# Kernel tuning notes

Measured on AMD Instinct MI355X. Metric: run time of the kernel, lower is better.

## Reference

```python
import jax, jax.numpy as jnp
import numpy as np

N_NODES = 100000
N_EDGES = 3200000
N_GRAPHS = 64


def gcn_conv(x, W, b, src, dst, num_nodes):
    # PyG GCNConv: h = x @ W; add self-loops; symmetric norm D^-1/2 (A+I) D^-1/2; bias after aggregation
    h = x @ W  # [N, out]
    loop = jnp.arange(num_nodes, dtype=src.dtype)
    src2 = jnp.concatenate([src, loop])
    dst2 = jnp.concatenate([dst, loop])
    deg = jax.ops.segment_sum(jnp.ones_like(src2, dtype=h.dtype), dst2, num_segments=num_nodes)
    dinv = jnp.where(deg > 0, jax.lax.rsqrt(jnp.maximum(deg, 1e-12)), 0.0)
    norm = dinv[src2] * dinv[dst2]  # [E+N]
    msg = h[src2] * norm[:, None]   # gather + scale (memory-bound)
    out = jax.ops.segment_sum(msg, dst2, num_segments=num_nodes)  # scatter-add
    return out + b


def global_mean_pool(x, batch, num_graphs):
    sums = jax.ops.segment_sum(x, batch, num_segments=num_graphs)
    cnts = jax.ops.segment_sum(jnp.ones((x.shape[0],), dtype=x.dtype), batch, num_segments=num_graphs)
    return sums / jnp.maximum(cnts, 1.0)[:, None]


def setup_inputs() -> dict:
    key = jax.random.key(0)
    ks = jax.random.split(key, 9)
    x = jax.random.normal(ks[0], (N_NODES, 1), dtype=jnp.float32)
    edge_index = jax.random.randint(ks[1], (2, N_EDGES), 0, N_NODES, dtype=jnp.int64)
    batch = jnp.sort(jax.random.randint(ks[2], (N_NODES,), 0, N_GRAPHS, dtype=jnp.int64))
    # Glorot-ish params
    W1 = jax.random.normal(ks[3], (1, 64), dtype=jnp.float32) * 0.5
    b1 = jnp.zeros((64,), dtype=jnp.float32)
    W2 = jax.random.normal(ks[4], (64, 32), dtype=jnp.float32) * (1.0 / np.sqrt(64))
    b2 = jnp.zeros((32,), dtype=jnp.float32)
    Wfc = jax.random.normal(ks[5], (32, 1), dtype=jnp.float32) * (1.0 / np.sqrt(32))
    bfc = jnp.zeros((1,), dtype=jnp.float32)
    return {"x": x, "edge_index": edge_index, "batch": batch,
            "W1": W1, "b1": b1, "W2": W2, "b2": b2, "Wfc": Wfc, "bfc": bfc}


def reference(x, edge_index, batch, W1, b1, W2, b2, Wfc, bfc):
    src, dst = edge_index[0], edge_index[1]
    h = jax.nn.relu(gcn_conv(x, W1, b1, src, dst, N_NODES))
    h = jax.nn.relu(gcn_conv(h, W2, b2, src, dst, N_NODES))
    g = global_mean_pool(h, batch, N_GRAPHS)  # [num_graphs, 32]
    return jax.nn.sigmoid(g @ Wfc + bfc)      # [num_graphs, 1]
```

## Files before the change

kernel.cpp:

```cpp
#include <hip/hip_runtime.h>
#include <math.h>

#define N_NODES 100000
#define N_EDGES 3200000
#define N_GRAPHS 64
#define BW 512
#define LSH 9
#define LMASK 511u
#define NBUCK ((N_NODES + BW - 1) / BW)
#define CHUNK_E 8192
#define NCHUNK ((N_EDGES + CHUNK_E - 1) / CHUNK_E)
#define POOL_SCALE 1024.0f
#define POOL_INV (1.0f / 1024.0f)
#define SENT ((unsigned int)N_NODES << LSH)

__global__ void k_count(const int* __restrict__ dst, unsigned int* __restrict__ counts,
                        unsigned int* __restrict__ totals) {
    __shared__ unsigned int h[NBUCK];
    for (int i = threadIdx.x; i < NBUCK; i += blockDim.x) h[i] = 0u;
    __syncthreads();
    int e0 = blockIdx.x * CHUNK_E;
    int e1 = min(e0 + CHUNK_E, N_EDGES);
    for (int e = e0 + threadIdx.x; e < e1; e += blockDim.x)
        atomicAdd(&h[dst[e] >> LSH], 1u);
    __syncthreads();
    for (int i = threadIdx.x; i < NBUCK; i += blockDim.x) {
        counts[(size_t)blockIdx.x * NBUCK + i] = h[i];
        if (h[i]) atomicAdd(&totals[i], h[i]);
    }
}

__global__ void k_scanc(unsigned int* __restrict__ counts, const unsigned int* __restrict__ totals,
                        unsigned int* __restrict__ base) {
    __shared__ unsigned int sd[1024];
    __shared__ unsigned int sbase;
    int bk = blockIdx.x;
    int t = threadIdx.x;
    unsigned int tv = (t < NBUCK) ? totals[t] : 0u;
    sd[t] = tv;
    __syncthreads();
    for (int o = 1; o < 1024; o <<= 1) {
        unsigned int x = (t >= o) ? sd[t - o] : 0u;
        __syncthreads();
        sd[t] += x;
        __syncthreads();
    }
    if (t == bk) {
        sbase = sd[t] - tv;
        base[bk] = sd[t] - tv;
        if (bk == 0) base[NBUCK] = N_EDGES;
    }
    __syncthreads();
    unsigned int v = (t < NCHUNK) ? counts[(size_t)t * NBUCK + bk] : 0u;
    sd[t] = v;
    __syncthreads();
    for (int o = 1; o < 1024; o <<= 1) {
        unsigned int x = (t >= o) ? sd[t - o] : 0u;
        __syncthreads();
        sd[t] += x;
        __syncthreads();
    }
    if (t < NCHUNK) counts[(size_t)t * NBUCK + bk] = sbase + sd[t] - v;
}

__global__ void k_part(const int* __restrict__ src, const int* __restrict__ dst,
                       const unsigned int* __restrict__ counts, unsigned int* __restrict__ packed) {
    __shared__ unsigned int sstart[NBUCK];
    __shared__ unsigned int lcur[NBUCK];
    for (int i = threadIdx.x; i < NBUCK; i += blockDim.x) {
        sstart[i] = counts[(size_t)blockIdx.x * NBUCK + i];
        lcur[i] = 0u;
    }
    __syncthreads();
    int e0 = blockIdx.x * CHUNK_E;
    int e1 = min(e0 + CHUNK_E, N_EDGES);
    for (int e = e0 + threadIdx.x; e < e1; e += blockDim.x) {
        int d = dst[e];
        int bk = d >> LSH;
        unsigned int pos = sstart[bk] + atomicAdd(&lcur[bk], 1u);
        packed[pos] = ((unsigned int)src[e] << LSH) | ((unsigned int)d & LMASK);
    }
}

__global__ void k_sort(const unsigned int* __restrict__ base, const unsigned int* __restrict__ packed,
                       unsigned int* __restrict__ packed2, unsigned int* __restrict__ rowstart) {
    __shared__ unsigned int hist[BW];
    __shared__ unsigned int scan[BW];
    __shared__ unsigned int cur[BW];
    int b = blockIdx.x;
    unsigned int e0 = base[b], e1 = base[b + 1];
    if (threadIdx.x < BW) hist[threadIdx.x] = 0u;
    __syncthreads();
    for (unsigned int e = e0 + threadIdx.x; e < e1; e += blockDim.x)
        atomicAdd(&hist[packed[e] & LMASK], 1u);
    __syncthreads();
    if (threadIdx.x < BW) scan[threadIdx.x] = hist[threadIdx.x];
    __syncthreads();
    for (int o = 1; o < BW; o <<= 1) {
        unsigned int v = 0u;
        if (threadIdx.x < BW && threadIdx.x >= (unsigned)o) v = scan[threadIdx.x - o];
        __syncthreads();
        if (threadIdx.x < BW && threadIdx.x >= (unsigned)o) scan[threadIdx.x] += v;
        __syncthreads();
    }
    if (threadIdx.x < BW) {
        unsigned int excl = scan[threadIdx.x] - hist[threadIdx.x];
        cur[threadIdx.x] = excl;
        rowstart[b * BW + threadIdx.x] = e0 + excl;
    }
    __syncthreads();
    for (unsigned int e = e0 + threadIdx.x; e < e1; e += blockDim.x) {
        unsigned int p = packed[e];
        unsigned int pos = e0 + atomicAdd(&cur[p & LMASK], 1u);
        packed2[pos] = p;
    }
}

__global__ void k_dinv(const unsigned int* __restrict__ rowstart, const float* __restrict__ x,
                       float* __restrict__ dinv, float* __restrict__ s, float2* __restrict__ ac) {
    int n = blockIdx.x * blockDim.x + threadIdx.x;
    if (n == 0) ac[N_NODES] = make_float2(0.0f, 0.0f);
    if (n < N_NODES) {
        unsigned int deg = rowstart[n + 1] - rowstart[n];
        float di = 1.0f / sqrtf((float)(deg + 1u));
        dinv[n] = di;
        s[n] = x[n] * di;
    }
}

__global__ void k_gcnt(const int* __restrict__ batch, float* __restrict__ gcnt) {
    __shared__ int lb[N_GRAPHS + 1];
    int b = threadIdx.x;
    if (b <= N_GRAPHS) {
        int lo = 0, hi = N_NODES;
        while (lo < hi) {
            int mid = (lo + hi) >> 1;
            if (batch[mid] < b) lo = mid + 1; else hi = mid;
        }
        lb[b] = lo;
    }
    __syncthreads();
    if (b < N_GRAPHS) gcnt[b] = (float)(lb[b + 1] - lb[b]);
}

#define NB1 16
__global__ void k_l1(const unsigned int* __restrict__ rowstart, const unsigned int* __restrict__ packed2,
                     const float* __restrict__ dinv, const float* __restrict__ s,
                     float2* __restrict__ ac) {
    int g = threadIdx.x >> 5, k = threadIdx.x & 31;
    int b = blockIdx.x;
    for (int d = g; d < NB1; d += 8) {
        int n = b * NB1 + d;
        if (n >= N_NODES) break;
        unsigned int rs = rowstart[n], re = rowstart[n + 1];
        float sum = 0.0f;
        for (unsigned int e = rs + k; e < re; e += 32)
            sum += s[packed2[e] >> LSH];
        sum += __shfl_xor(sum, 1);
        sum += __shfl_xor(sum, 2);
        sum += __shfl_xor(sum, 4);
        sum += __shfl_xor(sum, 8);
        sum += __shfl_xor(sum, 16);
        if (k == 0) {
            float di = dinv[n];
            ac[n] = make_float2(di, di * di * (sum + s[n]));
        }
    }
}

#define NPW 8

#define EDGE_PAIR(P) { \
    float4 q_ = Epair4[(P)]; \
    H += fmaxf(fmaf(q_.y, w1j, q_.x * b1j), 0.0f); \
    H += fmaxf(fmaf(q_.w, w1j, q_.z * b1j), 0.0f); }

#define BLOCK16(P0) { \
    EDGE_PAIR((P0) + 0) EDGE_PAIR((P0) + 1) EDGE_PAIR((P0) + 2) EDGE_PAIR((P0) + 3) \
    EDGE_PAIR((P0) + 4) EDGE_PAIR((P0) + 5) EDGE_PAIR((P0) + 6) EDGE_PAIR((P0) + 7) }

__global__ __launch_bounds__(256, 6)
void k_l2(const unsigned int* __restrict__ rowstart, const unsigned int* __restrict__ packed2,
          const float2* __restrict__ ac,
          const float* __restrict__ W1, const float* __restrict__ b1,
          const float* __restrict__ W2, const float* __restrict__ b2,
          const int* __restrict__ batch, int* __restrict__ gsumi) {
    __shared__ float Hrow[4][64];
    __shared__ float4 Ebuf[4][32];
    const int lane = threadIdx.x & 63;
    const int wv   = threadIdx.x >> 6;
    const int k    = lane & 31;
    const int jh   = lane >> 5;
    const int j0   = jh * 32;

    const float w1j = W1[lane];
    const float b1j = b1[lane];
    const float b2k = b2[k];
    float w2c[32];
#pragma unroll
    for (int j = 0; j < 32; j++) w2c[j] = W2[(j0 + j) * 32 + k];

    float4* Epair4 = &Ebuf[wv][0];
    float2* Ewr    = (float2*)&Ebuf[wv][0];

    int n0 = (blockIdx.x * 4 + wv) * NPW;
    float racc = 0.0f;
    int curg = -1;
    for (int i = 0; i < NPW; i++) {
        int n = n0 + i;
        if (n >= N_NODES) break;
        unsigned int rs = rowstart[n], re = rowstart[n + 1];
        float2 acn = ac[n];
        float H = fmaxf(fmaf(acn.y, w1j, acn.x * b1j), 0.0f);
        unsigned int e0 = rs;
        while (e0 + 64u <= re) {
            unsigned int p = packed2[e0 + lane];
            Ewr[lane] = ac[p >> LSH];
            BLOCK16(0) BLOCK16(8) BLOCK16(16) BLOCK16(24)
            e0 += 64u;
        }
        unsigned int rem = re - e0;
        if (rem) {
            unsigned int idx = e0 + lane;
            unsigned int p = SENT;
            if (idx < re) p = packed2[idx];
            Ewr[lane] = ac[p >> LSH];
            switch ((rem + 15u) >> 4) {
                case 4: BLOCK16(24); [[fallthrough]];
                case 3: BLOCK16(16); [[fallthrough]];
                case 2: BLOCK16(8);  [[fallthrough]];
                case 1: BLOCK16(0);
            }
        }
        Hrow[wv][lane] = H;
        float accv = 0.0f;
#pragma unroll
        for (int jj = 0; jj < 8; jj++) {
            float4 hv = *(const float4*)&Hrow[wv][j0 + 4 * jj];
            accv += hv.x * w2c[4 * jj + 0] + hv.y * w2c[4 * jj + 1]
                  + hv.z * w2c[4 * jj + 2] + hv.w * w2c[4 * jj + 3];
        }
        accv += __shfl_xor(accv, 32);
        float v = fmaxf(fmaf(acn.x, accv, b2k), 0.0f);
        int gb = batch[n];
        if (gb != curg) {
            if (curg >= 0 && jh == 0)
                atomicAdd(&gsumi[curg * 32 + k], __float2int_rn(racc * POOL_SCALE));
            racc = 0.0f; curg = gb;
        }
        racc += v;
    }
    if (curg >= 0 && jh == 0)
        atomicAdd(&gsumi[curg * 32 + k], __float2int_rn(racc * POOL_SCALE));
}

__global__ void k_readout(const int* __restrict__ gsumi, const float* __restrict__ gcnt,
                          const float* __restrict__ Wfc, const float* __restrict__ bfc,
                          float* __restrict__ out) {
    int b = threadIdx.x;
    if (b < N_GRAPHS) {
        float inv = 1.0f / fmaxf(gcnt[b], 1.0f);
        float acc = bfc[0];
#pragma unroll
        for (int k = 0; k < 32; k++)
            acc += (float)gsumi[b * 32 + k] * POOL_INV * inv * Wfc[k];
        out[b] = 1.0f / (1.0f + expf(-acc));
    }
}

extern "C" void kernel_launch(void* const* d_in, const int* in_sizes, int n_in,
                              void* d_out, int out_size, void* d_ws, size_t ws_size,
                              hipStream_t stream) {
    const float* x    = (const float*)d_in[0];
    const int*   ei   = (const int*)d_in[1];
    const int*   batch= (const int*)d_in[2];
    const float* W1   = (const float*)d_in[3];
    const float* b1   = (const float*)d_in[4];
    const float* W2   = (const float*)d_in[5];
    const float* b2   = (const float*)d_in[6];
    const float* Wfc  = (const float*)d_in[7];
    const float* bfc  = (const float*)d_in[8];
    float* out = (float*)d_out;

    const int* srcIdx = ei;
    const int* dstIdx = ei + N_EDGES;

    char* w = (char*)d_ws;
    unsigned int* totals  = (unsigned int*)w; w += ((NBUCK + 64) & ~63) * 4;
    unsigned int* base    = (unsigned int*)w; w += ((NBUCK + 1 + 63) & ~63) * 4;
    unsigned int* packed  = (unsigned int*)w; w += (size_t)N_EDGES * 4;
    unsigned int* packed2 = (unsigned int*)w; w += (size_t)(N_EDGES + 64) * 4;
    unsigned int* rowstart= (unsigned int*)w; w += (size_t)(NBUCK * BW + 64) * 4;
    float* dinv = (float*)w;                  w += (size_t)N_NODES * 4;
    float* sbuf = (float*)w;                  w += (size_t)N_NODES * 4;
    float2* ac  = (float2*)w;                 w += (size_t)(N_NODES + 8) * 8;
    int* gsumi  = (int*)w;                    w += (size_t)N_GRAPHS * 32 * 4;
    float* gcnt = (float*)w;                  w += (size_t)N_GRAPHS * 4;
    unsigned int* counts  = packed2;

    hipMemsetAsync(totals, 0, (size_t)NBUCK * 4, stream);
    hipMemsetAsync(gsumi, 0, (size_t)N_GRAPHS * 32 * 4, stream);

    k_count<<<NCHUNK, 512, 0, stream>>>(dstIdx, counts, totals);
    k_scanc<<<NBUCK, 1024, 0, stream>>>(counts, totals, base);
    k_part <<<NCHUNK, 512, 0, stream>>>(srcIdx, dstIdx, counts, packed);
    k_sort <<<NBUCK, 1024, 0, stream>>>(base, packed, packed2, rowstart);
    k_dinv <<<(N_NODES + 255) / 256, 256, 0, stream>>>(rowstart, x, dinv, sbuf, ac);
    k_gcnt <<<1, 128, 0, stream>>>(batch, gcnt);
    k_l1   <<<(N_NODES + NB1 - 1) / NB1, 256, 0, stream>>>(rowstart, packed2, dinv, sbuf, ac);
    k_l2   <<<(N_NODES + 4 * NPW - 1) / (4 * NPW), 256, 0, stream>>>(rowstart, packed2, ac, W1, b1, W2, b2, batch, gsumi);
    k_readout<<<1, 64, 0, stream>>>(gsumi, gcnt, Wfc, bfc, out);
}
```

Baseline: 229.0 us.

## Split bucket sort and fuse degree norm and layer-1 aggregation into it

```diff
diff --git a/kernel.cpp b/kernel.cpp
--- a/kernel.cpp
+++ b/kernel.cpp
@@ -82,14 +82,15 @@
     }
 }
 
-__global__ void k_sort(const unsigned int* __restrict__ base, const unsigned int* __restrict__ packed,
-                       unsigned int* __restrict__ packed2, unsigned int* __restrict__ rowstart) {
+__global__ void k_sorta(const unsigned int* __restrict__ base, const unsigned int* __restrict__ packed,
+                        unsigned int* __restrict__ rowstart, const float* __restrict__ x,
+                        float* __restrict__ dinv, float* __restrict__ s, float2* __restrict__ ac) {
     __shared__ unsigned int hist[BW];
     __shared__ unsigned int scan[BW];
-    __shared__ unsigned int cur[BW];
     int b = blockIdx.x;
     unsigned int e0 = base[b], e1 = base[b + 1];
     if (threadIdx.x < BW) hist[threadIdx.x] = 0u;
+    if (b == 0 && threadIdx.x == 0) ac[N_NODES] = make_float2(0.0f, 0.0f);
     __syncthreads();
     for (unsigned int e = e0 + threadIdx.x; e < e1; e += blockDim.x)
         atomicAdd(&hist[packed[e] & LMASK], 1u);
@@ -104,27 +105,45 @@
         __syncthreads();
     }
     if (threadIdx.x < BW) {
-        unsigned int excl = scan[threadIdx.x] - hist[threadIdx.x];
-        cur[threadIdx.x] = excl;
-        rowstart[b * BW + threadIdx.x] = e0 + excl;
+        unsigned int deg = hist[threadIdx.x];
+        rowstart[b * BW + threadIdx.x] = e0 + scan[threadIdx.x] - deg;
+        int n = b * BW + threadIdx.x;
+        if (n < N_NODES) {
+            float di = 1.0f / sqrtf((float)(deg + 1u));
+            dinv[n] = di;
+            s[n] = x[n] * di;
+        }
+    }
+}
+
+__global__ void k_sortb(const unsigned int* __restrict__ base, const unsigned int* __restrict__ packed,
+                        const unsigned int* __restrict__ rowstart,
+                        unsigned int* __restrict__ packed2,
+                        const float* __restrict__ dinv, const float* __restrict__ s,
+                        float2* __restrict__ ac) {
+    __shared__ unsigned int cur[BW];
+    __shared__ float fsum[BW];
+    int b = blockIdx.x;
+    unsigned int e0 = base[b], e1 = base[b + 1];
+    if (threadIdx.x < BW) {
+        cur[threadIdx.x] = rowstart[b * BW + threadIdx.x] - e0;
+        fsum[threadIdx.x] = 0.0f;
     }
     __syncthreads();
     for (unsigned int e = e0 + threadIdx.x; e < e1; e += blockDim.x) {
         unsigned int p = packed[e];
-        unsigned int pos = e0 + atomicAdd(&cur[p & LMASK], 1u);
+        unsigned int d = p & LMASK;
+        unsigned int pos = e0 + atomicAdd(&cur[d], 1u);
         packed2[pos] = p;
-    }
-}
-
-__global__ void k_dinv(const unsigned int* __restrict__ rowstart, const float* __restrict__ x,
-                       float* __restrict__ dinv, float* __restrict__ s, float2* __restrict__ ac) {
-    int n = blockIdx.x * blockDim.x + threadIdx.x;
-    if (n == 0) ac[N_NODES] = make_float2(0.0f, 0.0f);
-    if (n < N_NODES) {
-        unsigned int deg = rowstart[n + 1] - rowstart[n];
-        float di = 1.0f / sqrtf((float)(deg + 1u));
-        dinv[n] = di;
-        s[n] = x[n] * di;
+        atomicAdd(&fsum[d], s[p >> LSH]);
+    }
+    __syncthreads();
+    if (threadIdx.x < BW) {
+        int n = b * BW + threadIdx.x;
+        if (n < N_NODES) {
+            float di = dinv[n];
+            ac[n] = make_float2(di, di * di * (fsum[threadIdx.x] + s[n]));
+        }
     }
 }
 
@@ -141,31 +160,6 @@
     }
     __syncthreads();
     if (b < N_GRAPHS) gcnt[b] = (float)(lb[b + 1] - lb[b]);
-}
-
-#define NB1 16
-__global__ void k_l1(const unsigned int* __restrict__ rowstart, const unsigned int* __restrict__ packed2,
-                     const float* __restrict__ dinv, const float* __restrict__ s,
-                     float2* __restrict__ ac) {
-    int g = threadIdx.x >> 5, k = threadIdx.x & 31;
-    int b = blockIdx.x;
-    for (int d = g; d < NB1; d += 8) {
-        int n = b * NB1 + d;
-        if (n >= N_NODES) break;
-        unsigned int rs = rowstart[n], re = rowstart[n + 1];
-        float sum = 0.0f;
-        for (unsigned int e = rs + k; e < re; e += 32)
-            sum += s[packed2[e] >> LSH];
-        sum += __shfl_xor(sum, 1);
-        sum += __shfl_xor(sum, 2);
-        sum += __shfl_xor(sum, 4);
-        sum += __shfl_xor(sum, 8);
-        sum += __shfl_xor(sum, 16);
-        if (k == 0) {
-            float di = dinv[n];
-            ac[n] = make_float2(di, di * di * (sum + s[n]));
-        }
-    }
 }
 
 #define NPW 8
@@ -304,10 +298,9 @@
     k_count<<<NCHUNK, 512, 0, stream>>>(dstIdx, counts, totals);
     k_scanc<<<NBUCK, 1024, 0, stream>>>(counts, totals, base);
     k_part <<<NCHUNK, 512, 0, stream>>>(srcIdx, dstIdx, counts, packed);
-    k_sort <<<NBUCK, 1024, 0, stream>>>(base, packed, packed2, rowstart);
-    k_dinv <<<(N_NODES + 255) / 256, 256, 0, stream>>>(rowstart, x, dinv, sbuf, ac);
+    k_sorta<<<NBUCK, 1024, 0, stream>>>(base, packed, rowstart, x, dinv, sbuf, ac);
+    k_sortb<<<NBUCK, 1024, 0, stream>>>(base, packed, rowstart, packed2, dinv, sbuf, ac);
     k_gcnt <<<1, 128, 0, stream>>>(batch, gcnt);
-    k_l1   <<<(N_NODES + NB1 - 1) / NB1, 256, 0, stream>>>(rowstart, packed2, dinv, sbuf, ac);
     k_l2   <<<(N_NODES + 4 * NPW - 1) / (4 * NPW), 256, 0, stream>>>(rowstart, packed2, ac, W1, b1, W2, b2, batch, gsumi);
     k_readout<<<1, 64, 0, stream>>>(gsumi, gcnt, Wfc, bfc, out);
 }
```

Result: faster. 220.4 us (-3.8%).
